# Performance work log

Hardware: AMD Instinct MI355X
Metric: run time of the kernel (lower is better)

Reference implementation:

```python
import jax, jax.numpy as jnp
import numpy as np

B, C, W, D = 8, 512, 512, 8192  # batch, channels(input_dim), locations(width), output_dim


def setup_inputs() -> dict:
    key = jax.random.key(0)
    k1, k2 = jax.random.split(key)
    bottom1 = jax.random.normal(k1, (B, C, W), dtype=jnp.float32)
    bottom2 = jax.random.normal(k2, (B, C, W), dtype=jnp.float32)
    # Reproduce the module's default numpy-seeded sketch params exactly.
    np.random.seed(1); rand_h_1 = np.random.randint(D, size=C).astype(np.int64)
    np.random.seed(3); rand_s_1 = (2 * np.random.randint(2, size=C) - 1).astype(np.float32)
    np.random.seed(5); rand_h_2 = np.random.randint(D, size=C).astype(np.int64)
    np.random.seed(7); rand_s_2 = (2 * np.random.randint(2, size=C) - 1).astype(np.float32)
    return {
        "bottom1": bottom1, "bottom2": bottom2,
        "rand_h_1": jnp.asarray(rand_h_1), "rand_s_1": jnp.asarray(rand_s_1),
        "rand_h_2": jnp.asarray(rand_h_2), "rand_s_2": jnp.asarray(rand_s_2),
    }


def _count_sketch(flat, rand_h, rand_s, output_dim):
    # flat: [rows, C]; equivalent to flat @ dense_sketch_matrix but as a
    # signed scatter-add: column i of flat goes to output column rand_h[i].
    rows = flat.shape[0]
    signed = flat * rand_s[None, :]
    sketch = jnp.zeros((rows, output_dim), dtype=flat.dtype)
    return sketch.at[:, rand_h].add(signed)


def reference(bottom1, bottom2, rand_h_1, rand_s_1, rand_h_2, rand_s_2):
    batch, height, width = bottom1.shape
    out_dim = D
    flat1 = bottom1.transpose(0, 2, 1).reshape(-1, height)  # [B*W, C]
    flat2 = bottom2.transpose(0, 2, 1).reshape(-1, height)
    sk1 = _count_sketch(flat1, rand_h_1, rand_s_1, out_dim)
    sk2 = _count_sketch(flat2, rand_h_2, rand_s_2, out_dim)
    # circular convolution via FFT
    prod = jnp.fft.fft(sk1, axis=-1) * jnp.fft.fft(sk2, axis=-1)
    cbp_flat = jnp.fft.ifft(prod, axis=-1).real.astype(bottom1.dtype)
    return cbp_flat.reshape(batch, height, out_dim)
```

## Files before the change

### kernel.cpp

```cpp
#include <hip/hip_runtime.h>
#include <hip/hip_fp16.h>
#include <stdint.h>

#define CBP_D 8192
#define CBP_C 512
#define CBP_W 512
#define ROWS 64
#define NTHREADS 1024
#define NSPLIT 4
#define NCAP 72

#define X1OFF 65664
#define PADW  (512u << 17)

__global__ __launch_bounds__(512, 2)
void pB_fill(const int* __restrict__ h1, const int* __restrict__ h2,
             int* __restrict__ cnt, uint32_t* __restrict__ pairs) {
    __shared__ int sc[CBP_D];
    __shared__ int sb[CBP_D];
    __shared__ int ssum[512];
    __shared__ short sbk[CBP_C];
    __shared__ int sh1[CBP_C];
    __shared__ int sh2[CBP_C];
    __shared__ int pc[64][8];
    __shared__ int rawt[64];
    int tid = threadIdx.x;

    for (int k = tid; k < CBP_D; k += 512) sc[k] = 0;
    sh1[tid] = h1[tid];
    sh2[tid] = h2[tid];
    __syncthreads();
    atomicAdd(&sc[sh2[tid]], 1);
    __syncthreads();
    int base = tid * 16;
    int loc[16]; int s = 0;
#pragma unroll
    for (int k = 0; k < 16; ++k) { loc[k] = sc[base + k]; s += loc[k]; }
    ssum[tid] = s;
    __syncthreads();
    int acc = s;
    for (int off = 1; off < 512; off <<= 1) {
        int add = (tid >= off) ? ssum[tid - off] : 0;
        __syncthreads();
        acc += add; ssum[tid] = acc;
        __syncthreads();
    }
    int excl = acc - s;
#pragma unroll
    for (int k = 0; k < 16; ++k) { sb[base + k] = excl; excl += loc[k]; }
    __syncthreads();
    {
        int h = sh2[tid]; int r = 0;
        for (int j2 = 0; j2 < tid; ++j2) r += (sh2[j2] == h);
        sbk[sb[h] + r] = (short)tid;
    }
    __syncthreads();

    int dl = tid >> 3, p = tid & 7;
    int d = blockIdx.x * 64 + dl;
    int i0 = p << 6;
    int cp = 0;
#pragma unroll 4
    for (int i = i0; i < i0 + 64; ++i) cp += sc[(d - sh1[i]) & (CBP_D - 1)];
    pc[dl][p] = cp;
    __syncthreads();
    int off = 0, tot = 0;
#pragma unroll
    for (int p2 = 0; p2 < 8; ++p2) { int v = pc[dl][p2]; off += (p2 < p) ? v : 0; tot += v; }
    uint32_t* pd = pairs + (size_t)d * NCAP;
    int pos = off;
    for (int i = i0; i < i0 + 64; ++i) {
        int t = (d - sh1[i]) & (CBP_D - 1);
        int n = sc[t];
        if (n) {
            int bo = sb[t];
            uint32_t iw = (uint32_t)(i << 7);
            for (int k = 0; k < n; ++k)
                pd[pos++] = iw | ((uint32_t)sbk[bo + k] << 17);
        }
    }
    if (p == 0) rawt[dl] = tot;
    __syncthreads();
    int q = dl & ~3;
    int qmax = max(max(rawt[q], rawt[q + 1]), max(rawt[q + 2], rawt[q + 3]));
    qmax = (qmax + 3) & ~3;
    for (int pos2 = tot + p; pos2 < qmax; pos2 += 8) pd[pos2] = PADW;
    if (p == 0) cnt[d] = qmax;
}


#define PROC(P) { \
    uint32_t p_ = (P); \
    uint32_t aB_ = (p_ & 0x1FF80u) + baseA; \
    uint32_t bB_ = ((p_ >> 10) & 0x1FF80u) | baseB; \
    uint2 ra_ = *(const uint2*)(xsh + aB_); \
    uint2 rb_ = *(const uint2*)(xsh + bB_); \
    a01 = __hfma2(*(const __half2*)&ra_.x, *(const __half2*)&rb_.x, a01); \
    a23 = __hfma2(*(const __half2*)&ra_.y, *(const __half2*)&rb_.y, a23); }

#define QUAD(K, DEST) { \
    int q_ = (qq << 2) + (K); \
    int quadbase_ = dbase + (q_ << 2); \
    int nmax_ = nmax_cur; \
    uint4 cur_ = pp_cur; \
    int nq_ = (q_ + 1 < 32) ? q_ + 1 : 31; \
    int nmax_n_ = __builtin_amdgcn_readfirstlane(cnt[dbase + (nq_ << 2)]); \
    uint4 pp_n_ = *(const uint4*)(pairs + (size_t)(dbase + (nq_ << 2) + g4) * NCAP); \
    const uint4* pl4_ = (const uint4*)(pairs + (size_t)(quadbase_ + g4) * NCAP); \
    float ac0 = 0.f, ac1 = 0.f, ac2 = 0.f, ac3 = 0.f; \
    int nb_ = nmax_ >> 2; \
    int t4_ = 0; \
    while (t4_ < nb_) { \
        __half2 a01 = __floats2half2_rn(0.f, 0.f); \
        __half2 a23 = __floats2half2_rn(0.f, 0.f); \
        int ce_ = (t4_ + 4 < nb_) ? t4_ + 4 : nb_; \
        for (; t4_ < ce_; ++t4_) { \
            uint4 c_ = cur_; \
            int nxt_ = (t4_ + 1 < nb_) ? t4_ + 1 : t4_; \
            cur_ = pl4_[nxt_]; \
            PROC(c_.x); PROC(c_.y); PROC(c_.z); PROC(c_.w); \
        } \
        float2 u_ = __half22float2(a01); ac0 += u_.x; ac1 += u_.y; \
        float2 v_ = __half22float2(a23); ac2 += v_.x; ac3 += v_.y; \
    } \
    nmax_cur = nmax_n_; pp_cur = pp_n_; \
    float s0_ = __shfl_xor(ac0, 16, 64), s1_ = __shfl_xor(ac1, 16, 64); \
    float s2_ = __shfl_xor(ac2, 16, 64), s3_ = __shfl_xor(ac3, 16, 64); \
    bool ge1_ = (g4 & 1) == 0; \
    float n0_ = ge1_ ? ac0 : s1_, n1_ = ge1_ ? s0_ : ac1; \
    float n2_ = ge1_ ? ac2 : s3_, n3_ = ge1_ ? s2_ : ac3; \
    s0_ = __shfl_xor(n0_, 32, 64); s1_ = __shfl_xor(n1_, 32, 64); \
    s2_ = __shfl_xor(n2_, 32, 64); s3_ = __shfl_xor(n3_, 32, 64); \
    bool ge2_ = (g4 & 2) == 0; \
    DEST = make_float4(ge2_ ? n0_ : s2_, ge2_ ? n1_ : s3_, \
                       ge2_ ? s0_ : n2_, ge2_ ? s1_ : n3_); }

__global__ __launch_bounds__(NTHREADS, 4)
void k_main(const float* __restrict__ b1, const float* __restrict__ b2,
            const float* __restrict__ s1, const float* __restrict__ s2,
            const int* __restrict__ cnt, const uint32_t* __restrict__ pairs,
            float* __restrict__ out) {
    __shared__ __align__(16) char xsh[131200];
    int bx = blockIdx.x;
    int gy = blockIdx.y;
    int r_base = bx * ROWS;
    int b = r_base >> 9;
    int w0 = r_base & (CBP_W - 1);
    int tid = threadIdx.x;

    for (int u = tid; u < CBP_C * 8; u += NTHREADS) {
        int c = u >> 3;
        int r8 = (u & 7) << 3;
        size_t g = ((size_t)(b * CBP_C + c)) * CBP_W + w0 + r8;
        float4 u0 = *(const float4*)(b1 + g), u1 = *(const float4*)(b1 + g + 4);
        float4 v0 = *(const float4*)(b2 + g), v1 = *(const float4*)(b2 + g + 4);
        float sa = s1[c], sb = s2[c];
        union { __half2 h2[4]; uint4 q; } A, Bv;
        A.h2[0] = __floats2half2_rn(u0.x * sa, u0.y * sa);
        A.h2[1] = __floats2half2_rn(u0.z * sa, u0.w * sa);
        A.h2[2] = __floats2half2_rn(u1.x * sa, u1.y * sa);
        A.h2[3] = __floats2half2_rn(u1.z * sa, u1.w * sa);
        Bv.h2[0] = __floats2half2_rn(v0.x * sb, v0.y * sb);
        Bv.h2[1] = __floats2half2_rn(v0.z * sb, v0.w * sb);
        Bv.h2[2] = __floats2half2_rn(v1.x * sb, v1.y * sb);
        Bv.h2[3] = __floats2half2_rn(v1.z * sb, v1.w * sb);
        *(uint4*)(xsh + X1OFF + (c << 7) + (r8 << 1)) = A.q;
        *(uint4*)(xsh + (c << 7) + (r8 << 1)) = Bv.q;
    }
    if (tid < 8) *(uint4*)(xsh + 65536 + tid * 16) = make_uint4(0, 0, 0, 0);
    __syncthreads();

    int wv = tid >> 6;
    int lane = tid & 63;
    int g4 = lane >> 4;
    int l = lane & 15;
    uint32_t baseA = (uint32_t)(X1OFF + (l << 3));
    uint32_t baseB = (uint32_t)(l << 3);
    int dbase = gy * (CBP_D / NSPLIT) + wv * 128;

    int nmax_cur = __builtin_amdgcn_readfirstlane(cnt[dbase]);
    uint4 pp_cur = *(const uint4*)(pairs + (size_t)(dbase + g4) * NCAP);

    float* obase = out + (size_t)(r_base + (l << 2) + g4) * CBP_D + dbase;

    for (int qq = 0; qq < 8; ++qq) {
        float4 B0, B1, B2, B3;
        QUAD(0, B0); QUAD(1, B1); QUAD(2, B2); QUAD(3, B3);
        float* o_ = obase + (qq << 4);
        *(float4*)(o_)      = B0;
        *(float4*)(o_ + 4)  = B1;
        *(float4*)(o_ + 8)  = B2;
        *(float4*)(o_ + 12) = B3;
    }
}


extern "C" void kernel_launch(void* const* d_in, const int* in_sizes, int n_in,
                              void* d_out, int out_size, void* d_ws, size_t ws_size,
                              hipStream_t stream) {
    const float* b1 = (const float*)d_in[0];
    const float* b2 = (const float*)d_in[1];
    const int*   h1 = (const int*)d_in[2];
    const float* s1 = (const float*)d_in[3];
    const int*   h2 = (const int*)d_in[4];
    const float* s2 = (const float*)d_in[5];
    float* out = (float*)d_out;

    int* cnt = (int*)d_ws;
    uint32_t* pairs = (uint32_t*)(cnt + 8192 + 8);

    pB_fill<<<128, 512, 0, stream>>>(h1, h2, cnt, pairs);

    dim3 g(CBP_W * 8 / ROWS, NSPLIT);
    k_main<<<g, NTHREADS, 0, stream>>>(b1, b2, s1, s2, cnt, pairs, out);
}
```

Baseline: 152.3 us.

## Halve row tile to 32, process 8 outputs per wave group with padded LDS

Cuts the rows per block from 64 to 32, which halves the LDS footprint and allows 8 blocks per CU instead of 4. Each wave now handles octets of 8 output columns with 8-lane groups. The LDS row stride is padded to 72 bytes to spread bank accesses, so the pair encoding stores scaled indices. The shuffle-based output transpose is rewritten for the new lane mapping. Padding is now computed over groups of 8 outputs, which may add wasted padded pairs, and each block stages less input per unit of work, so there is less data reuse.

```diff
diff --git a/kernel.cpp b/kernel.cpp
--- a/kernel.cpp
+++ b/kernel.cpp
@@ -5,13 +5,15 @@
 #define CBP_D 8192
 #define CBP_C 512
 #define CBP_W 512
-#define ROWS 64
+#define ROWS 32
 #define NTHREADS 1024
 #define NSPLIT 4
 #define NCAP 72
 
-#define X1OFF 65664
-#define PADW  (512u << 17)
+#define X1OFF 36936
+#define ZOFF  36864
+#define PADW  ((uint32_t)4608u << 16)
+#define LDSSZ 73800
 
 __global__ __launch_bounds__(512, 2)
 void pB_fill(const int* __restrict__ h1, const int* __restrict__ h2,
@@ -74,39 +76,41 @@
         int n = sc[t];
         if (n) {
             int bo = sb[t];
-            uint32_t iw = (uint32_t)(i << 7);
+            uint32_t iw = (uint32_t)(i * 9);
             for (int k = 0; k < n; ++k)
-                pd[pos++] = iw | ((uint32_t)sbk[bo + k] << 17);
+                pd[pos++] = iw | ((uint32_t)((int)sbk[bo + k] * 9) << 16);
         }
     }
     if (p == 0) rawt[dl] = tot;
     __syncthreads();
-    int q = dl & ~3;
-    int qmax = max(max(rawt[q], rawt[q + 1]), max(rawt[q + 2], rawt[q + 3]));
-    qmax = (qmax + 3) & ~3;
-    for (int pos2 = tot + p; pos2 < qmax; pos2 += 8) pd[pos2] = PADW;
-    if (p == 0) cnt[d] = qmax;
+    int q = dl & ~7;
+    int omax = 0;
+#pragma unroll
+    for (int z = 0; z < 8; ++z) omax = max(omax, rawt[q + z]);
+    omax = (omax + 3) & ~3;
+    for (int pos2 = tot + p; pos2 < omax; pos2 += 8) pd[pos2] = PADW;
+    if (p == 0) cnt[d] = omax;
 }
 
 
 #define PROC(P) { \
     uint32_t p_ = (P); \
-    uint32_t aB_ = (p_ & 0x1FF80u) + baseA; \
-    uint32_t bB_ = ((p_ >> 10) & 0x1FF80u) | baseB; \
+    uint32_t aB_ = ((p_ & 0xFFFFu) << 3) + baseA; \
+    uint32_t bB_ = ((p_ >> 16) << 3) + baseB; \
     uint2 ra_ = *(const uint2*)(xsh + aB_); \
     uint2 rb_ = *(const uint2*)(xsh + bB_); \
     a01 = __hfma2(*(const __half2*)&ra_.x, *(const __half2*)&rb_.x, a01); \
     a23 = __hfma2(*(const __half2*)&ra_.y, *(const __half2*)&rb_.y, a23); }
 
-#define QUAD(K, DEST) { \
-    int q_ = (qq << 2) + (K); \
-    int quadbase_ = dbase + (q_ << 2); \
+#define OCT(K, DEST) { \
+    int oc_ = (oo << 1) + (K); \
+    int octb_ = dbase + (oc_ << 3); \
     int nmax_ = nmax_cur; \
     uint4 cur_ = pp_cur; \
-    int nq_ = (q_ + 1 < 32) ? q_ + 1 : 31; \
-    int nmax_n_ = __builtin_amdgcn_readfirstlane(cnt[dbase + (nq_ << 2)]); \
-    uint4 pp_n_ = *(const uint4*)(pairs + (size_t)(dbase + (nq_ << 2) + g4) * NCAP); \
-    const uint4* pl4_ = (const uint4*)(pairs + (size_t)(quadbase_ + g4) * NCAP); \
+    int no_ = (oc_ + 1 < 16) ? oc_ + 1 : 15; \
+    int nmax_n_ = __builtin_amdgcn_readfirstlane(cnt[dbase + (no_ << 3)]); \
+    uint4 pp_n_ = *(const uint4*)(pairs + (size_t)(dbase + (no_ << 3) + grp) * NCAP); \
+    const uint4* pl4_ = (const uint4*)(pairs + (size_t)(octb_ + grp) * NCAP); \
     float ac0 = 0.f, ac1 = 0.f, ac2 = 0.f, ac3 = 0.f; \
     int nb_ = nmax_ >> 2; \
     int t4_ = 0; \
@@ -124,23 +128,27 @@
         float2 v_ = __half22float2(a23); ac2 += v_.x; ac3 += v_.y; \
     } \
     nmax_cur = nmax_n_; pp_cur = pp_n_; \
-    float s0_ = __shfl_xor(ac0, 16, 64), s1_ = __shfl_xor(ac1, 16, 64); \
-    float s2_ = __shfl_xor(ac2, 16, 64), s3_ = __shfl_xor(ac3, 16, 64); \
-    bool ge1_ = (g4 & 1) == 0; \
-    float n0_ = ge1_ ? ac0 : s1_, n1_ = ge1_ ? s0_ : ac1; \
-    float n2_ = ge1_ ? ac2 : s3_, n3_ = ge1_ ? s2_ : ac3; \
-    s0_ = __shfl_xor(n0_, 32, 64); s1_ = __shfl_xor(n1_, 32, 64); \
-    s2_ = __shfl_xor(n2_, 32, 64); s3_ = __shfl_xor(n3_, 32, 64); \
-    bool ge2_ = (g4 & 2) == 0; \
-    DEST = make_float4(ge2_ ? n0_ : s2_, ge2_ ? n1_ : s3_, \
-                       ge2_ ? s0_ : n2_, ge2_ ? s1_ : n3_); }
-
-__global__ __launch_bounds__(NTHREADS, 4)
+    float v0_, v1_, v2_, v3_; \
+    { float u0_ = __shfl(ac0, srcb, 64), u1_ = __shfl(ac1, srcb, 64); \
+      float u2_ = __shfl(ac2, srcb, 64), u3_ = __shfl(ac3, srcb, 64); \
+      v0_ = kk == 0 ? u0_ : kk == 1 ? u1_ : kk == 2 ? u2_ : u3_; } \
+    { float u0_ = __shfl(ac0, srcb + 8, 64), u1_ = __shfl(ac1, srcb + 8, 64); \
+      float u2_ = __shfl(ac2, srcb + 8, 64), u3_ = __shfl(ac3, srcb + 8, 64); \
+      v1_ = kk == 0 ? u0_ : kk == 1 ? u1_ : kk == 2 ? u2_ : u3_; } \
+    { float u0_ = __shfl(ac0, srcb + 16, 64), u1_ = __shfl(ac1, srcb + 16, 64); \
+      float u2_ = __shfl(ac2, srcb + 16, 64), u3_ = __shfl(ac3, srcb + 16, 64); \
+      v2_ = kk == 0 ? u0_ : kk == 1 ? u1_ : kk == 2 ? u2_ : u3_; } \
+    { float u0_ = __shfl(ac0, srcb + 24, 64), u1_ = __shfl(ac1, srcb + 24, 64); \
+      float u2_ = __shfl(ac2, srcb + 24, 64), u3_ = __shfl(ac3, srcb + 24, 64); \
+      v3_ = kk == 0 ? u0_ : kk == 1 ? u1_ : kk == 2 ? u2_ : u3_; } \
+    DEST = make_float4(v0_, v1_, v2_, v3_); }
+
+__global__ __launch_bounds__(NTHREADS, 8)
 void k_main(const float* __restrict__ b1, const float* __restrict__ b2,
             const float* __restrict__ s1, const float* __restrict__ s2,
             const int* __restrict__ cnt, const uint32_t* __restrict__ pairs,
             float* __restrict__ out) {
-    __shared__ __align__(16) char xsh[131200];
+    __shared__ __align__(16) char xsh[LDSSZ];
     int bx = blockIdx.x;
     int gy = blockIdx.y;
     int r_base = bx * ROWS;
@@ -148,9 +156,9 @@
     int w0 = r_base & (CBP_W - 1);
     int tid = threadIdx.x;
 
-    for (int u = tid; u < CBP_C * 8; u += NTHREADS) {
-        int c = u >> 3;
-        int r8 = (u & 7) << 3;
+    for (int u = tid; u < CBP_C * 4; u += NTHREADS) {
+        int c = u >> 2;
+        int r8 = (u & 3) << 3;
         size_t g = ((size_t)(b * CBP_C + c)) * CBP_W + w0 + r8;
         float4 u0 = *(const float4*)(b1 + g), u1 = *(const float4*)(b1 + g + 4);
         float4 v0 = *(const float4*)(b2 + g), v1 = *(const float4*)(b2 + g + 4);
@@ -164,33 +172,37 @@
         Bv.h2[1] = __floats2half2_rn(v0.z * sb, v0.w * sb);
         Bv.h2[2] = __floats2half2_rn(v1.x * sb, v1.y * sb);
         Bv.h2[3] = __floats2half2_rn(v1.z * sb, v1.w * sb);
-        *(uint4*)(xsh + X1OFF + (c << 7) + (r8 << 1)) = A.q;
-        *(uint4*)(xsh + (c << 7) + (r8 << 1)) = Bv.q;
-    }
-    if (tid < 8) *(uint4*)(xsh + 65536 + tid * 16) = make_uint4(0, 0, 0, 0);
+        char* pA = xsh + X1OFF + c * 72 + (r8 << 1);
+        char* pB = xsh + c * 72 + (r8 << 1);
+        *(uint2*)pA       = make_uint2(A.q.x, A.q.y);
+        *(uint2*)(pA + 8) = make_uint2(A.q.z, A.q.w);
+        *(uint2*)pB       = make_uint2(Bv.q.x, Bv.q.y);
+        *(uint2*)(pB + 8) = make_uint2(Bv.q.z, Bv.q.w);
+    }
+    if (tid < 8) *(uint2*)(xsh + ZOFF + tid * 8) = make_uint2(0, 0);
     __syncthreads();
 
     int wv = tid >> 6;
     int lane = tid & 63;
-    int g4 = lane >> 4;
-    int l = lane & 15;
+    int grp = lane >> 3;
+    int l = lane & 7;
     uint32_t baseA = (uint32_t)(X1OFF + (l << 3));
     uint32_t baseB = (uint32_t)(l << 3);
     int dbase = gy * (CBP_D / NSPLIT) + wv * 128;
+    int rr = lane & 31, dq = lane >> 5, kk = rr & 3;
+    int srcb = (dq << 5) + (rr >> 2);
 
     int nmax_cur = __builtin_amdgcn_readfirstlane(cnt[dbase]);
-    uint4 pp_cur = *(const uint4*)(pairs + (size_t)(dbase + g4) * NCAP);
-
-    float* obase = out + (size_t)(r_base + (l << 2) + g4) * CBP_D + dbase;
-
-    for (int qq = 0; qq < 8; ++qq) {
-        float4 B0, B1, B2, B3;
-        QUAD(0, B0); QUAD(1, B1); QUAD(2, B2); QUAD(3, B3);
-        float* o_ = obase + (qq << 4);
-        *(float4*)(o_)      = B0;
-        *(float4*)(o_ + 4)  = B1;
-        *(float4*)(o_ + 8)  = B2;
-        *(float4*)(o_ + 12) = B3;
+    uint4 pp_cur = *(const uint4*)(pairs + (size_t)(dbase + grp) * NCAP);
+
+    float* obase = out + (size_t)(r_base + rr) * CBP_D + dbase + (dq << 2);
+
+    for (int oo = 0; oo < 8; ++oo) {
+        float4 B0, B1;
+        OCT(0, B0); OCT(1, B1);
+        float* o_ = obase + (oo << 4);
+        *(float4*)(o_)     = B0;
+        *(float4*)(o_ + 8) = B1;
     }
 }
 
```

After: 156.4 us. +2.7%, slower.

## Process eight output columns per lane group with 16-byte LDS loads

Applied to the files above, without the earlier changes.

The main kernel now splits each wavefront into eight groups of eight lanes instead of four groups of sixteen. Each lane handles eight rows with 128-bit LDS loads and four half2 accumulators, and a three-stage shuffle transpose replaces the two-stage one. Padding in the pair-building kernel now rounds to the maximum over eight output columns instead of four, so padding overhead grows. The aim is fewer LDS load instructions per FMA and fewer index decodes per pair, at the cost of more registers, more shuffles and more padded work.

```diff
diff --git a/kernel.cpp b/kernel.cpp
--- a/kernel.cpp
+++ b/kernel.cpp
@@ -11,6 +11,7 @@
 #define NCAP 72
 
 #define X1OFF 65664
+#define ZOFF  65536
 #define PADW  (512u << 17)
 
 __global__ __launch_bounds__(512, 2)
@@ -81,38 +82,43 @@
     }
     if (p == 0) rawt[dl] = tot;
     __syncthreads();
-    int q = dl & ~3;
-    int qmax = max(max(rawt[q], rawt[q + 1]), max(rawt[q + 2], rawt[q + 3]));
-    qmax = (qmax + 3) & ~3;
-    for (int pos2 = tot + p; pos2 < qmax; pos2 += 8) pd[pos2] = PADW;
-    if (p == 0) cnt[d] = qmax;
+    int q = dl & ~7;
+    int omax = 0;
+#pragma unroll
+    for (int z = 0; z < 8; ++z) omax = max(omax, rawt[q + z]);
+    omax = (omax + 3) & ~3;
+    for (int pos2 = tot + p; pos2 < omax; pos2 += 8) pd[pos2] = PADW;
+    if (p == 0) cnt[d] = omax;
 }
 
 
 #define PROC(P) { \
     uint32_t p_ = (P); \
     uint32_t aB_ = (p_ & 0x1FF80u) + baseA; \
-    uint32_t bB_ = ((p_ >> 10) & 0x1FF80u) | baseB; \
-    uint2 ra_ = *(const uint2*)(xsh + aB_); \
-    uint2 rb_ = *(const uint2*)(xsh + bB_); \
+    uint32_t bB_ = ((p_ >> 10) & 0x1FF80u) + baseB; \
+    uint4 ra_ = *(const uint4*)(xsh + aB_); \
+    uint4 rb_ = *(const uint4*)(xsh + bB_); \
     a01 = __hfma2(*(const __half2*)&ra_.x, *(const __half2*)&rb_.x, a01); \
-    a23 = __hfma2(*(const __half2*)&ra_.y, *(const __half2*)&rb_.y, a23); }
-
-#define QUAD(K, DEST) { \
-    int q_ = (qq << 2) + (K); \
-    int quadbase_ = dbase + (q_ << 2); \
+    a23 = __hfma2(*(const __half2*)&ra_.y, *(const __half2*)&rb_.y, a23); \
+    a45 = __hfma2(*(const __half2*)&ra_.z, *(const __half2*)&rb_.z, a45); \
+    a67 = __hfma2(*(const __half2*)&ra_.w, *(const __half2*)&rb_.w, a67); }
+
+#define OCT(K, DST0, DST1) { \
+    int oc_ = (oo << 1) + (K); \
+    int octb_ = dbase + (oc_ << 3); \
     int nmax_ = nmax_cur; \
     uint4 cur_ = pp_cur; \
-    int nq_ = (q_ + 1 < 32) ? q_ + 1 : 31; \
-    int nmax_n_ = __builtin_amdgcn_readfirstlane(cnt[dbase + (nq_ << 2)]); \
-    uint4 pp_n_ = *(const uint4*)(pairs + (size_t)(dbase + (nq_ << 2) + g4) * NCAP); \
-    const uint4* pl4_ = (const uint4*)(pairs + (size_t)(quadbase_ + g4) * NCAP); \
-    float ac0 = 0.f, ac1 = 0.f, ac2 = 0.f, ac3 = 0.f; \
+    int no_ = (oc_ + 1 < 16) ? oc_ + 1 : 15; \
+    int nmax_n_ = __builtin_amdgcn_readfirstlane(cnt[dbase + (no_ << 3)]); \
+    uint4 pp_n_ = *(const uint4*)(pairs + (size_t)(dbase + (no_ << 3) + grp) * NCAP); \
+    const uint4* pl4_ = (const uint4*)(pairs + (size_t)(octb_ + grp) * NCAP); \
+    float f0 = 0.f, f1 = 0.f, f2 = 0.f, f3 = 0.f; \
+    float f4 = 0.f, f5 = 0.f, f6 = 0.f, f7 = 0.f; \
     int nb_ = nmax_ >> 2; \
     int t4_ = 0; \
     while (t4_ < nb_) { \
         __half2 a01 = __floats2half2_rn(0.f, 0.f); \
-        __half2 a23 = __floats2half2_rn(0.f, 0.f); \
+        __half2 a23 = a01, a45 = a01, a67 = a01; \
         int ce_ = (t4_ + 4 < nb_) ? t4_ + 4 : nb_; \
         for (; t4_ < ce_; ++t4_) { \
             uint4 c_ = cur_; \
@@ -120,20 +126,36 @@
             cur_ = pl4_[nxt_]; \
             PROC(c_.x); PROC(c_.y); PROC(c_.z); PROC(c_.w); \
         } \
-        float2 u_ = __half22float2(a01); ac0 += u_.x; ac1 += u_.y; \
-        float2 v_ = __half22float2(a23); ac2 += v_.x; ac3 += v_.y; \
+        float2 u_; \
+        u_ = __half22float2(a01); f0 += u_.x; f1 += u_.y; \
+        u_ = __half22float2(a23); f2 += u_.x; f3 += u_.y; \
+        u_ = __half22float2(a45); f4 += u_.x; f5 += u_.y; \
+        u_ = __half22float2(a67); f6 += u_.x; f7 += u_.y; \
     } \
     nmax_cur = nmax_n_; pp_cur = pp_n_; \
-    float s0_ = __shfl_xor(ac0, 16, 64), s1_ = __shfl_xor(ac1, 16, 64); \
-    float s2_ = __shfl_xor(ac2, 16, 64), s3_ = __shfl_xor(ac3, 16, 64); \
-    bool ge1_ = (g4 & 1) == 0; \
-    float n0_ = ge1_ ? ac0 : s1_, n1_ = ge1_ ? s0_ : ac1; \
-    float n2_ = ge1_ ? ac2 : s3_, n3_ = ge1_ ? s2_ : ac3; \
-    s0_ = __shfl_xor(n0_, 32, 64); s1_ = __shfl_xor(n1_, 32, 64); \
-    s2_ = __shfl_xor(n2_, 32, 64); s3_ = __shfl_xor(n3_, 32, 64); \
-    bool ge2_ = (g4 & 2) == 0; \
-    DEST = make_float4(ge2_ ? n0_ : s2_, ge2_ ? n1_ : s3_, \
-                       ge2_ ? s0_ : n2_, ge2_ ? s1_ : n3_); }
+     \
+    { float t0 = __shfl_xor(f1, 8, 64), t1 = __shfl_xor(f0, 8, 64); \
+      float t2 = __shfl_xor(f3, 8, 64), t3 = __shfl_xor(f2, 8, 64); \
+      float t4 = __shfl_xor(f5, 8, 64), t5 = __shfl_xor(f4, 8, 64); \
+      float t6 = __shfl_xor(f7, 8, 64), t7 = __shfl_xor(f6, 8, 64); \
+      f0 = h0 ? t0 : f0; f1 = h0 ? f1 : t1; f2 = h0 ? t2 : f2; f3 = h0 ? f3 : t3; \
+      f4 = h0 ? t4 : f4; f5 = h0 ? f5 : t5; f6 = h0 ? t6 : f6; f7 = h0 ? f7 : t7; } \
+     \
+    { float t0 = __shfl_xor(f2, 16, 64), t1 = __shfl_xor(f3, 16, 64); \
+      float t2 = __shfl_xor(f0, 16, 64), t3 = __shfl_xor(f1, 16, 64); \
+      float t4 = __shfl_xor(f6, 16, 64), t5 = __shfl_xor(f7, 16, 64); \
+      float t6 = __shfl_xor(f4, 16, 64), t7 = __shfl_xor(f5, 16, 64); \
+      f0 = h1 ? t0 : f0; f1 = h1 ? t1 : f1; f2 = h1 ? f2 : t2; f3 = h1 ? f3 : t3; \
+      f4 = h1 ? t4 : f4; f5 = h1 ? t5 : f5; f6 = h1 ? f6 : t6; f7 = h1 ? f7 : t7; } \
+     \
+    { float t0 = __shfl_xor(f4, 32, 64), t1 = __shfl_xor(f5, 32, 64); \
+      float t2 = __shfl_xor(f6, 32, 64), t3 = __shfl_xor(f7, 32, 64); \
+      float t4 = __shfl_xor(f0, 32, 64), t5 = __shfl_xor(f1, 32, 64); \
+      float t6 = __shfl_xor(f2, 32, 64), t7 = __shfl_xor(f3, 32, 64); \
+      f0 = h2 ? t0 : f0; f1 = h2 ? t1 : f1; f2 = h2 ? t2 : f2; f3 = h2 ? t3 : f3; \
+      f4 = h2 ? f4 : t4; f5 = h2 ? f5 : t5; f6 = h2 ? f6 : t6; f7 = h2 ? f7 : t7; } \
+    DST0 = make_float4(f0, f1, f2, f3); \
+    DST1 = make_float4(f4, f5, f6, f7); }
 
 __global__ __launch_bounds__(NTHREADS, 4)
 void k_main(const float* __restrict__ b1, const float* __restrict__ b2,
@@ -167,26 +189,28 @@
         *(uint4*)(xsh + X1OFF + (c << 7) + (r8 << 1)) = A.q;
         *(uint4*)(xsh + (c << 7) + (r8 << 1)) = Bv.q;
     }
-    if (tid < 8) *(uint4*)(xsh + 65536 + tid * 16) = make_uint4(0, 0, 0, 0);
+    if (tid < 8) *(uint4*)(xsh + ZOFF + tid * 16) = make_uint4(0, 0, 0, 0);
     __syncthreads();
 
     int wv = tid >> 6;
     int lane = tid & 63;
-    int g4 = lane >> 4;
-    int l = lane & 15;
-    uint32_t baseA = (uint32_t)(X1OFF + (l << 3));
-    uint32_t baseB = (uint32_t)(l << 3);
+    int grp = lane >> 3;
+    int l = lane & 7;
+    bool h0 = (grp & 1) != 0, h1 = (grp & 2) != 0, h2 = (grp & 4) != 0;
+    uint32_t baseA = (uint32_t)(X1OFF + (l << 4));
+    uint32_t baseB = (uint32_t)(l << 4);
     int dbase = gy * (CBP_D / NSPLIT) + wv * 128;
 
     int nmax_cur = __builtin_amdgcn_readfirstlane(cnt[dbase]);
-    uint4 pp_cur = *(const uint4*)(pairs + (size_t)(dbase + g4) * NCAP);
-
-    float* obase = out + (size_t)(r_base + (l << 2) + g4) * CBP_D + dbase;
-
-    for (int qq = 0; qq < 8; ++qq) {
+    uint4 pp_cur = *(const uint4*)(pairs + (size_t)(dbase + grp) * NCAP);
+
+    int rrow = (l << 3) + grp;
+    float* obase = out + (size_t)(r_base + rrow) * CBP_D + dbase;
+
+    for (int oo = 0; oo < 8; ++oo) {
         float4 B0, B1, B2, B3;
-        QUAD(0, B0); QUAD(1, B1); QUAD(2, B2); QUAD(3, B3);
-        float* o_ = obase + (qq << 4);
+        OCT(0, B0, B1); OCT(1, B2, B3);
+        float* o_ = obase + (oo << 4);
         *(float4*)(o_)      = B0;
         *(float4*)(o_ + 4)  = B1;
         *(float4*)(o_ + 8)  = B2;
```

Result: faster. 134.0 us (-12.0%).
